# Kernel optimization log

Hardware: AMD Instinct MI355X
Metric: run time of the kernel (lower is better)

The kernel has to match this reference:

```python
import jax, jax.numpy as jnp
import numpy as np

DIM = 4096
N_HEADS = 32
N_KV_HEADS = 8
HEAD_DIM = 128
WINDOW = 4096
BATCH = 32
START_POS = 4095


def setup_inputs() -> dict:
    key = jax.random.key(0)
    ks = jax.random.split(key, 8)
    x = jax.random.normal(ks[0], (BATCH, DIM), dtype=jnp.float32)
    wqkv = jax.random.normal(ks[1], (DIM, (N_HEADS + 2 * N_KV_HEADS) * HEAD_DIM), dtype=jnp.float32) * 0.02
    wo = jax.random.normal(ks[2], (N_HEADS * HEAD_DIM, DIM), dtype=jnp.float32) * 0.02
    cos = jax.random.uniform(ks[3], (HEAD_DIM,), dtype=jnp.float32)
    sin = jax.random.uniform(ks[4], (HEAD_DIM,), dtype=jnp.float32)
    cache_k = jax.random.normal(ks[5], (BATCH, N_KV_HEADS, WINDOW, HEAD_DIM), dtype=jnp.float32)
    cache_v = jax.random.normal(ks[6], (BATCH, N_KV_HEADS, WINDOW, HEAD_DIM), dtype=jnp.float32)
    mask = jnp.zeros((BATCH, 1, 1, WINDOW), dtype=jnp.float32)
    return {"x": x, "wqkv": wqkv, "wo": wo, "cos": cos, "sin": sin,
            "cache_k": cache_k, "cache_v": cache_v, "mask": mask,
            "start_pos": START_POS}


def _rotate_half(t):
    t1, t2 = jnp.split(t, 2, axis=-1)
    return jnp.concatenate([-t2, t1], axis=-1)


def _rope(t, cos, sin):
    # t: [..., head_dim]; cos/sin: [head_dim] at the current decode position
    return t * cos + _rotate_half(t) * sin


def reference(x, wqkv, wo, cos, sin, cache_k, cache_v, mask, start_pos):
    B, D = x.shape
    KV = cache_k.shape[1]
    Hd = cache_k.shape[3]
    window = cache_k.shape[2]
    H = wo.shape[0] // Hd
    R = H // KV  # GQA repeats
    scale = 1.0 / np.sqrt(Hd)

    # fused QKV projection (matmul_1d + nlp_create_qkv_heads)
    qkv = x @ wqkv  # [B, (H+2*KV)*Hd]
    q = qkv[:, : H * Hd].reshape(B, H, Hd)
    k = qkv[:, H * Hd : (H + KV) * Hd].reshape(B, KV, Hd)
    v = qkv[:, (H + KV) * Hd :].reshape(B, KV, Hd)

    # rotary embedding on q and k at current position
    q = _rope(q, cos, sin)
    k = _rope(k, cos, sin)

    # sliding-window KV cache update at current_pos
    cur = start_pos % window  # python int
    cache_k = cache_k.at[:, :, cur].set(k)
    cache_v = cache_v.at[:, :, cur].set(v)

    # unpad to padded_layer_past_len = min(nearest_32(start_pos+1), window)
    padded_len = min(((start_pos + 1 + 31) // 32) * 32, window)
    keys = cache_k[:, :, :padded_len]   # [B, KV, T, Hd]
    values = cache_v[:, :, :padded_len]

    # grouped-query attention: q -> [B, KV, R, Hd]
    qg = q.reshape(B, KV, R, Hd)
    scores = jnp.einsum("bgrd,bgtd->bgrt", qg, keys) * scale  # [B, KV, R, T]
    scores = scores + mask[:, :, :, :padded_len]  # broadcast over kv-heads/repeats
    attn = jax.nn.softmax(scores, axis=-1)
    out = jnp.einsum("bgrt,bgtd->bgrd", attn, values)  # [B, KV, R, Hd]

    # concat heads + output projection
    out = out.reshape(B, H * Hd)
    return out @ wo  # [B, D]
```

## Files before the change

### kernel.cpp

```cpp
#include <hip/hip_runtime.h>
#include <math.h>

#define DIM 4096
#define NH 32
#define NKV 8
#define HD 128
#define WINDOW 4096
#define BATCH 32
#define QKV_N 6144
#define ATTN_SCALE 0.08838834764831845f
#define CHUNK 512
#define NC 8
#define SLICES 8

__device__ __forceinline__ float4 f4max(float4 a, float4 b) {
  return make_float4(fmaxf(a.x, b.x), fmaxf(a.y, b.y), fmaxf(a.z, b.z), fmaxf(a.w, b.w));
}
__device__ __forceinline__ float4 f4add(float4 a, float4 b) {
  return make_float4(a.x + b.x, a.y + b.y, a.z + b.z, a.w + b.w);
}
__device__ __forceinline__ void fma4(float4& a, float4 x, float4 y) {
  a.x = fmaf(x.x, y.x, a.x); a.y = fmaf(x.y, y.y, a.y);
  a.z = fmaf(x.z, y.z, a.z); a.w = fmaf(x.w, y.w, a.w);
}
__device__ __forceinline__ void fma4s(float4& a, float s, float4 v) {
  a.x = fmaf(s, v.x, a.x); a.y = fmaf(s, v.y, a.y);
  a.z = fmaf(s, v.z, a.z); a.w = fmaf(s, v.w, a.w);
}

template<int N, int K, int NS>
__global__ __launch_bounds__(256)
void gemm_part(const float* __restrict__ x, const float* __restrict__ w,
               float* __restrict__ part) {
  const int t = threadIdx.x;
  const int c0 = blockIdx.x * 64 + (t & 15) * 4;
  const int r0 = (t >> 4) * 2;
  const int kn = K / NS;
  const int ks = blockIdx.y * kn;

  float a00 = 0.f, a01 = 0.f, a02 = 0.f, a03 = 0.f;
  float a10 = 0.f, a11 = 0.f, a12 = 0.f, a13 = 0.f;

  const float* xr0 = x + (size_t)r0 * K;
  const float* xr1 = xr0 + K;
  const float* wp = w + (size_t)ks * N + c0;

  for (int k = ks; k < ks + kn; k += 4) {
    float4 xa = *(const float4*)(xr0 + k);
    float4 xb = *(const float4*)(xr1 + k);
    float xav[4] = {xa.x, xa.y, xa.z, xa.w};
    float xbv[4] = {xb.x, xb.y, xb.z, xb.w};
#pragma unroll
    for (int kk = 0; kk < 4; ++kk) {
      float4 wv = *(const float4*)(wp);
      wp += N;
      a00 = fmaf(xav[kk], wv.x, a00);
      a01 = fmaf(xav[kk], wv.y, a01);
      a02 = fmaf(xav[kk], wv.z, a02);
      a03 = fmaf(xav[kk], wv.w, a03);
      a10 = fmaf(xbv[kk], wv.x, a10);
      a11 = fmaf(xbv[kk], wv.y, a11);
      a12 = fmaf(xbv[kk], wv.z, a12);
      a13 = fmaf(xbv[kk], wv.w, a13);
    }
  }
  float* p = part + ((size_t)blockIdx.y * 32 + r0) * N + c0;
  *(float4*)p = make_float4(a00, a01, a02, a03);
  *(float4*)(p + N) = make_float4(a10, a11, a12, a13);
}

__global__ __launch_bounds__(256)
void rope_reduce(const float* __restrict__ part, const float* __restrict__ cosv,
                 const float* __restrict__ sinv, float* __restrict__ q,
                 float* __restrict__ knew, float* __restrict__ vnew) {
  int idx = blockIdx.x * 256 + threadIdx.x;
  int r = idx / 3072;
  int rem = idx - r * 3072;
  int head = rem >> 6;
  int d = rem & 63;
  int c1 = head * 128 + d;
  int c2 = c1 + 64;
  float v1 = 0.f, v2 = 0.f;
#pragma unroll
  for (int s = 0; s < SLICES; ++s) {
    v1 += part[((size_t)s * 32 + r) * QKV_N + c1];
    v2 += part[((size_t)s * 32 + r) * QKV_N + c2];
  }
  if (head < NH + NKV) {
    float c_lo = cosv[d], c_hi = cosv[d + 64];
    float s_lo = sinv[d], s_hi = sinv[d + 64];
    float o1 = v1 * c_lo - v2 * s_lo;
    float o2 = v2 * c_hi + v1 * s_hi;
    if (head < NH) {
      q[((size_t)r * NH + head) * HD + d] = o1;
      q[((size_t)r * NH + head) * HD + d + 64] = o2;
    } else {
      int g = head - NH;
      knew[((size_t)r * NKV + g) * HD + d] = o1;
      knew[((size_t)r * NKV + g) * HD + d + 64] = o2;
    }
  } else {
    int g = head - NH - NKV;
    vnew[((size_t)r * NKV + g) * HD + d] = v1;
    vnew[((size_t)r * NKV + g) * HD + d + 64] = v2;
  }
}

__global__ __launch_bounds__(256)
void attn_chunk(const float* __restrict__ q, const float* __restrict__ knew,
                const float* __restrict__ vnew, const float* __restrict__ cache_k,
                const float* __restrict__ cache_v, const float* __restrict__ mask,
                const int* __restrict__ start_pos_p,
                float* __restrict__ pvp, float* __restrict__ msp) {
  const int bg = blockIdx.x;
  const int b = bg >> 3;
  const int c = blockIdx.y;
  const int t = threadIdx.x;
  const int sp = start_pos_p[0];
  const int cur = sp & (WINDOW - 1);
  int plen = ((sp + 1 + 31) >> 5) << 5;
  if (plen > WINDOW) plen = WINDOW;
  const int t0 = c * CHUNK;
  const int tend = min(t0 + CHUNK, plen);

  const size_t msbase = (((size_t)c * 256 + bg) * 4) * 2;
  float* pvb = pvp + (((size_t)c * 256 + bg) * 4) * HD;

  __shared__ __align__(16) float q_s[4][HD];
  __shared__ __align__(16) float s_lds[CHUNK][4];
  __shared__ float4 scratch4[1024];
  float* scratch = (float*)scratch4;

  if (t0 >= plen) {
    if (t < 8) msp[msbase + t] = (t & 1) ? 0.f : -1e30f;
    for (int i = t; i < 4 * HD; i += 256) pvb[i] = 0.f;
    return;
  }

  for (int i = t; i < 512; i += 256) {
    int h = i >> 7, d = i & 127;
    q_s[h][d] = q[((size_t)b * NH + ((bg & 7) * 4 + h)) * HD + d];
  }
  __syncthreads();

  const float* kbase = cache_k + (size_t)bg * WINDOW * HD;
  const float* vbase = cache_v + (size_t)bg * WINDOW * HD;
  const float* krow_new = knew + (size_t)bg * HD;
  const float* vrow_new = vnew + (size_t)bg * HD;

  {
    const int p0 = t >> 2;
    const int dl = t & 3;
    for (int tt = t0 + p0; tt < t0 + CHUNK; tt += 64) {
      if (tt < tend) {
        const float* krow = (tt == cur) ? krow_new : (kbase + (size_t)tt * HD);
        float4 a0 = {0,0,0,0}, a1 = {0,0,0,0}, a2 = {0,0,0,0}, a3 = {0,0,0,0};
#pragma unroll
        for (int j = 0; j < 8; ++j) {
          const int f = dl + 4 * j;
          float4 kv = *(const float4*)(krow + 4 * f);
          fma4(a0, kv, *(const float4*)(&q_s[0][4 * f]));
          fma4(a1, kv, *(const float4*)(&q_s[1][4 * f]));
          fma4(a2, kv, *(const float4*)(&q_s[2][4 * f]));
          fma4(a3, kv, *(const float4*)(&q_s[3][4 * f]));
        }
        float s0 = a0.x + a0.y + a0.z + a0.w;
        float s1 = a1.x + a1.y + a1.z + a1.w;
        float s2 = a2.x + a2.y + a2.z + a2.w;
        float s3 = a3.x + a3.y + a3.z + a3.w;
        s0 += __shfl_xor(s0, 1); s0 += __shfl_xor(s0, 2);
        s1 += __shfl_xor(s1, 1); s1 += __shfl_xor(s1, 2);
        s2 += __shfl_xor(s2, 1); s2 += __shfl_xor(s2, 2);
        s3 += __shfl_xor(s3, 1); s3 += __shfl_xor(s3, 2);
        float sv = (dl == 0) ? s0 : (dl == 1) ? s1 : (dl == 2) ? s2 : s3;
        s_lds[tt - t0][dl] = sv * ATTN_SCALE + mask[(size_t)b * WINDOW + tt];
      } else {
        s_lds[tt - t0][dl] = -1e30f;
      }
    }
  }
  __syncthreads();

  float4* red4 = scratch4;
  float4 lmax = {-1e30f, -1e30f, -1e30f, -1e30f};
  for (int i = t; i < CHUNK; i += 256) lmax = f4max(lmax, *(const float4*)(s_lds[i]));
  red4[t] = lmax;
  __syncthreads();
  for (int s = 128; s > 0; s >>= 1) {
    if (t < s) red4[t] = f4max(red4[t], red4[t + s]);
    __syncthreads();
  }
  float4 mx = red4[0];
  __syncthreads();

  float4 lsum = {0, 0, 0, 0};
  for (int i = t; i < CHUNK; i += 256) {
    float4 s = *(const float4*)(s_lds[i]);
    s.x = __expf(s.x - mx.x);
    s.y = __expf(s.y - mx.y);
    s.z = __expf(s.z - mx.z);
    s.w = __expf(s.w - mx.w);
    *(float4*)(s_lds[i]) = s;
    lsum = f4add(lsum, s);
  }
  red4[t] = lsum;
  __syncthreads();
  for (int s = 128; s > 0; s >>= 1) {
    if (t < s) red4[t] = f4add(red4[t], red4[t + s]);
    __syncthreads();
  }
  if (t == 0) {
    float4 sm = red4[0];
    msp[msbase + 0] = mx.x; msp[msbase + 1] = sm.x;
    msp[msbase + 2] = mx.y; msp[msbase + 3] = sm.y;
    msp[msbase + 4] = mx.z; msp[msbase + 5] = sm.z;
    msp[msbase + 6] = mx.w; msp[msbase + 7] = sm.w;
  }
  __syncthreads();

  {
    const int d4 = t & 31;
    const int toff = t >> 5;
    float4 a0 = {0,0,0,0}, a1 = {0,0,0,0}, a2 = {0,0,0,0}, a3 = {0,0,0,0};
    for (int tt = t0 + toff; tt < tend; tt += 8) {
      const float* vrow = (tt == cur) ? vrow_new : (vbase + (size_t)tt * HD);
      float4 vv = *(const float4*)(vrow + 4 * d4);
      float4 p = *(const float4*)(s_lds[tt - t0]);
      fma4s(a0, p.x, vv);
      fma4s(a1, p.y, vv);
      fma4s(a2, p.z, vv);
      fma4s(a3, p.w, vv);
    }
    *(float4*)(&scratch[(toff * 4 + 0) * HD + 4 * d4]) = a0;
    *(float4*)(&scratch[(toff * 4 + 1) * HD + 4 * d4]) = a1;
    *(float4*)(&scratch[(toff * 4 + 2) * HD + 4 * d4]) = a2;
    *(float4*)(&scratch[(toff * 4 + 3) * HD + 4 * d4]) = a3;
  }
  __syncthreads();
  for (int i = t; i < 4 * HD; i += 256) {
    float s = 0.f;
#pragma unroll
    for (int o = 0; o < 8; ++o) s += scratch[o * 512 + i];
    pvb[i] = s;
  }
}

__global__ __launch_bounds__(256)
void attn_combine(const float* __restrict__ pvp, const float* __restrict__ msp,
                  float* __restrict__ attn_out) {
  int idx = blockIdx.x * 256 + threadIdx.x;
  int b = idx >> 12;
  int rem = idx & 4095;
  int hf = rem >> 7;
  int d = rem & 127;
  int g = hf >> 2, hh = hf & 3;
  int bg = b * 8 + g;
  float mv[NC], sv[NC];
  float M = -1e30f;
#pragma unroll
  for (int c = 0; c < NC; ++c) {
    mv[c] = msp[(((size_t)c * 256 + bg) * 4 + hh) * 2];
    sv[c] = msp[(((size_t)c * 256 + bg) * 4 + hh) * 2 + 1];
    M = fmaxf(M, mv[c]);
  }
  float num = 0.f, den = 0.f;
#pragma unroll
  for (int c = 0; c < NC; ++c) {
    float w = __expf(mv[c] - M);
    den = fmaf(sv[c], w, den);
    num = fmaf(pvp[(((size_t)c * 256 + bg) * 4 + hh) * HD + d], w, num);
  }
  attn_out[idx] = num / den;
}

__global__ __launch_bounds__(256)
void reduce_out(const float* __restrict__ part, float* __restrict__ out) {
  int idx = blockIdx.x * 256 + threadIdx.x;
  float s = 0.f;
#pragma unroll
  for (int sl = 0; sl < SLICES; ++sl) s += part[(size_t)sl * 32 * DIM + idx];
  out[idx] = s;
}

extern "C" void kernel_launch(void* const* d_in, const int* in_sizes, int n_in,
                              void* d_out, int out_size, void* d_ws, size_t ws_size,
                              hipStream_t stream) {
  const float* x       = (const float*)d_in[0];
  const float* wqkv    = (const float*)d_in[1];
  const float* wo      = (const float*)d_in[2];
  const float* cosv    = (const float*)d_in[3];
  const float* sinv    = (const float*)d_in[4];
  const float* cache_k = (const float*)d_in[5];
  const float* cache_v = (const float*)d_in[6];
  const float* mask    = (const float*)d_in[7];
  const int*   start_p = (const int*)d_in[8];
  float* ws = (float*)d_ws;

  float* part     = ws;
  float* q        = ws + 1572864;
  float* knew     = q + 131072;
  float* vnew     = knew + 32768;
  float* attn_out = vnew + 32768;
  float* pvp      = attn_out + 131072;
  float* msp      = pvp + 1048576;
  float* out      = (float*)d_out;

  gemm_part<QKV_N, DIM, SLICES><<<dim3(QKV_N / 64, SLICES), 256, 0, stream>>>(x, wqkv, part);
  rope_reduce<<<384, 256, 0, stream>>>(part, cosv, sinv, q, knew, vnew);
  attn_chunk<<<dim3(BATCH * NKV, NC), 256, 0, stream>>>(q, knew, vnew, cache_k,
                                                        cache_v, mask, start_p,
                                                        pvp, msp);
  attn_combine<<<512, 256, 0, stream>>>(pvp, msp, attn_out);
  gemm_part<DIM, DIM, SLICES><<<dim3(DIM / 64, SLICES), 256, 0, stream>>>(attn_out, wo, part);
  reduce_out<<<512, 256, 0, stream>>>(part, out);
}
```

Measured before the change: 368.1 us.

## Double attention chunks and GEMM K-slices; use wave-shuffle softmax reductions

After: 364.2 us. About the same (-1.0%).

```diff
diff --git a/kernel.cpp b/kernel.cpp
--- a/kernel.cpp
+++ b/kernel.cpp
@@ -9,9 +9,9 @@
 #define BATCH 32
 #define QKV_N 6144
 #define ATTN_SCALE 0.08838834764831845f
-#define CHUNK 512
-#define NC 8
-#define SLICES 8
+#define CHUNK 256
+#define NC 16
+#define SLICES 16
 
 __device__ __forceinline__ float4 f4max(float4 a, float4 b) {
   return make_float4(fmaxf(a.x, b.x), fmaxf(a.y, b.y), fmaxf(a.z, b.z), fmaxf(a.w, b.w));
@@ -26,6 +26,26 @@
 __device__ __forceinline__ void fma4s(float4& a, float s, float4 v) {
   a.x = fmaf(s, v.x, a.x); a.y = fmaf(s, v.y, a.y);
   a.z = fmaf(s, v.z, a.z); a.w = fmaf(s, v.w, a.w);
+}
+__device__ __forceinline__ float4 wred_max(float4 v) {
+#pragma unroll
+  for (int o = 1; o < 64; o <<= 1) {
+    v.x = fmaxf(v.x, __shfl_xor(v.x, o));
+    v.y = fmaxf(v.y, __shfl_xor(v.y, o));
+    v.z = fmaxf(v.z, __shfl_xor(v.z, o));
+    v.w = fmaxf(v.w, __shfl_xor(v.w, o));
+  }
+  return v;
+}
+__device__ __forceinline__ float4 wred_add(float4 v) {
+#pragma unroll
+  for (int o = 1; o < 64; o <<= 1) {
+    v.x += __shfl_xor(v.x, o);
+    v.y += __shfl_xor(v.y, o);
+    v.z += __shfl_xor(v.z, o);
+    v.w += __shfl_xor(v.w, o);
+  }
+  return v;
 }
 
 template<int N, int K, int NS>
@@ -116,6 +136,7 @@
   const int b = bg >> 3;
   const int c = blockIdx.y;
   const int t = threadIdx.x;
+  const int w = t >> 6;
   const int sp = start_pos_p[0];
   const int cur = sp & (WINDOW - 1);
   int plen = ((sp + 1 + 31) >> 5) << 5;
@@ -128,8 +149,8 @@
 
   __shared__ __align__(16) float q_s[4][HD];
   __shared__ __align__(16) float s_lds[CHUNK][4];
-  __shared__ float4 scratch4[1024];
-  float* scratch = (float*)scratch4;
+  __shared__ __align__(16) float4 red_s[8];
+  __shared__ __align__(16) float scratch[8 * 512];
 
   if (t0 >= plen) {
     if (t < 8) msp[msbase + t] = (t & 1) ? 0.f : -1e30f;
@@ -181,42 +202,28 @@
   }
   __syncthreads();
 
-  float4* red4 = scratch4;
-  float4 lmax = {-1e30f, -1e30f, -1e30f, -1e30f};
-  for (int i = t; i < CHUNK; i += 256) lmax = f4max(lmax, *(const float4*)(s_lds[i]));
-  red4[t] = lmax;
-  __syncthreads();
-  for (int s = 128; s > 0; s >>= 1) {
-    if (t < s) red4[t] = f4max(red4[t], red4[t + s]);
-    __syncthreads();
-  }
-  float4 mx = red4[0];
-  __syncthreads();
-
-  float4 lsum = {0, 0, 0, 0};
-  for (int i = t; i < CHUNK; i += 256) {
-    float4 s = *(const float4*)(s_lds[i]);
-    s.x = __expf(s.x - mx.x);
-    s.y = __expf(s.y - mx.y);
-    s.z = __expf(s.z - mx.z);
-    s.w = __expf(s.w - mx.w);
-    *(float4*)(s_lds[i]) = s;
-    lsum = f4add(lsum, s);
-  }
-  red4[t] = lsum;
-  __syncthreads();
-  for (int s = 128; s > 0; s >>= 1) {
-    if (t < s) red4[t] = f4add(red4[t], red4[t + s]);
-    __syncthreads();
-  }
+  float4 sval = *(const float4*)(s_lds[t]);
+  float4 m = wred_max(sval);
+  if ((t & 63) == 0) red_s[w] = m;
+  __syncthreads();
+  float4 mx = f4max(f4max(red_s[0], red_s[1]), f4max(red_s[2], red_s[3]));
+
+  float4 e;
+  e.x = __expf(sval.x - mx.x);
+  e.y = __expf(sval.y - mx.y);
+  e.z = __expf(sval.z - mx.z);
+  e.w = __expf(sval.w - mx.w);
+  *(float4*)(s_lds[t]) = e;
+  float4 s = wred_add(e);
+  if ((t & 63) == 0) red_s[4 + w] = s;
+  __syncthreads();
   if (t == 0) {
-    float4 sm = red4[0];
+    float4 sm = f4add(f4add(red_s[4], red_s[5]), f4add(red_s[6], red_s[7]));
     msp[msbase + 0] = mx.x; msp[msbase + 1] = sm.x;
     msp[msbase + 2] = mx.y; msp[msbase + 3] = sm.y;
     msp[msbase + 4] = mx.z; msp[msbase + 5] = sm.z;
     msp[msbase + 6] = mx.w; msp[msbase + 7] = sm.w;
   }
-  __syncthreads();
 
   {
     const int d4 = t & 31;
@@ -238,10 +245,10 @@
   }
   __syncthreads();
   for (int i = t; i < 4 * HD; i += 256) {
-    float s = 0.f;
-#pragma unroll
-    for (int o = 0; o < 8; ++o) s += scratch[o * 512 + i];
-    pvb[i] = s;
+    float s2 = 0.f;
+#pragma unroll
+    for (int o = 0; o < 8; ++o) s2 += scratch[o * 512 + i];
+    pvb[i] = s2;
   }
 }
 
@@ -297,12 +304,12 @@
   float* ws = (float*)d_ws;
 
   float* part     = ws;
-  float* q        = ws + 1572864;
+  float* q        = ws + 3145728;
   float* knew     = q + 131072;
   float* vnew     = knew + 32768;
   float* attn_out = vnew + 32768;
   float* pvp      = attn_out + 131072;
-  float* msp      = pvp + 1048576;
+  float* msp      = pvp + 2097152;
   float* out      = (float*)d_out;
 
   gemm_part<QKV_N, DIM, SLICES><<<dim3(QKV_N / 64, SLICES), 256, 0, stream>>>(x, wqkv, part);
```
